# Optimization experiments

Hardware: AMD Instinct MI355X
Metric: run time of the kernel (lower is better)

Reference implementation:

```python
import jax, jax.numpy as jnp
import numpy as np

NUM_HEADS = 16
HEAD_DIM = 64

def setup_inputs() -> dict:
    key = jax.random.key(0)
    k1, k2, k3 = jax.random.split(key, 3)
    B, S, H = 2, 2048, 1024
    inner = NUM_HEADS * HEAD_DIM  # 1024
    x = jax.random.normal(k1, (B, S, H), dtype=jnp.float32)
    w_qkv = jax.random.normal(k2, (H, 3 * inner), dtype=jnp.float32) * (1.0 / np.sqrt(H))
    b_qkv = jnp.zeros((3 * inner,), dtype=jnp.float32)
    w_out = jax.random.normal(k3, (inner, H), dtype=jnp.float32) * (1.0 / np.sqrt(inner))
    b_out = jnp.zeros((H,), dtype=jnp.float32)
    return {"x": x, "w_qkv": w_qkv, "b_qkv": b_qkv, "w_out": w_out, "b_out": b_out}

def reference(x, w_qkv, b_qkv, w_out, b_out):
    B, S, H = x.shape
    nh, hd = NUM_HEADS, HEAD_DIM
    qkv = x @ w_qkv + b_qkv                      # [B,S,3*nh*hd]
    qkv = qkv.reshape(B, S, 3, nh, hd)
    qkv = jnp.transpose(qkv, (2, 0, 3, 1, 4))    # [3,B,nh,S,hd]
    q, k, v = qkv[0], qkv[1], qkv[2]
    scale = jnp.sqrt(jnp.asarray(hd, dtype=x.dtype))
    attn = jnp.einsum('bhqd,bhkd->bhqk', q, k) / scale  # [B,nh,S,S]
    attn = jax.nn.softmax(attn, axis=-1)
    out = jnp.einsum('bhqk,bhkd->bhqd', attn, v)        # [B,nh,S,hd]
    out = jnp.transpose(out, (0, 2, 1, 3)).reshape(B, S, nh * hd)
    out = out @ w_out + b_out                    # [B,S,H]
    return out
```

## Files before the change

### kernel.cpp

```cpp
#include <hip/hip_runtime.h>
#include <stdint.h>

typedef short bf16x8 __attribute__((ext_vector_type(8)));
typedef float f32x4 __attribute__((ext_vector_type(4)));

#if __has_builtin(__builtin_amdgcn_exp2f)
#define EXP2F(x) __builtin_amdgcn_exp2f(x)
#else
#define EXP2F(x) exp2f(x)
#endif

#define QSCALE 0.18033688011112042f

__device__ __forceinline__ unsigned short f2bf(float f) {
  unsigned u = __float_as_uint(f);
  u += 0x7fffu + ((u >> 16) & 1u);
  return (unsigned short)(u >> 16);
}

__device__ __forceinline__ unsigned cvtpk(float lo, float hi) {
  unsigned r;
  asm("v_cvt_pk_bf16_f32 %0, %1, %2" : "=v"(r) : "v"(lo), "v"(hi));
  return r;
}

__device__ __forceinline__ void gld16(const ushort* g, ushort* l) {
  __builtin_amdgcn_global_load_lds(
      (__attribute__((address_space(1))) void*)g,
      (__attribute__((address_space(3))) void*)l, 16, 0, 0);
}

__global__ __launch_bounds__(256) void k_cast_bf16(const float* __restrict__ in,
                                                   ushort* __restrict__ out) {
  int i = (blockIdx.x * 256 + threadIdx.x) * 8;
  float4 a = *(const float4*)(in + i);
  float4 b = *(const float4*)(in + i + 4);
  union { ushort u[8]; uint4 q; } r;
  r.u[0] = f2bf(a.x); r.u[1] = f2bf(a.y); r.u[2] = f2bf(a.z); r.u[3] = f2bf(a.w);
  r.u[4] = f2bf(b.x); r.u[5] = f2bf(b.y); r.u[6] = f2bf(b.z); r.u[7] = f2bf(b.w);
  *(uint4*)(out + i) = r.q;
}

__global__ __launch_bounds__(256) void k_transpose_cast(const float* __restrict__ in,
                                                        ushort* __restrict__ out,
                                                        int R, int C) {
  __shared__ float tl[32][33];
  int t = threadIdx.x;
  {
    int r = t >> 3, c4 = (t & 7) * 4;
    float4 v = *(const float4*)(in + (size_t)(blockIdx.y * 32 + r) * C + blockIdx.x * 32 + c4);
    tl[r][c4] = v.x; tl[r][c4 + 1] = v.y; tl[r][c4 + 2] = v.z; tl[r][c4 + 3] = v.w;
  }
  __syncthreads();
  {
    int c = t >> 3, r4 = (t & 7) * 4;
    union { ushort u[4]; uint2 q; } o;
    o.u[0] = f2bf(tl[r4][c]);     o.u[1] = f2bf(tl[r4 + 1][c]);
    o.u[2] = f2bf(tl[r4 + 2][c]); o.u[3] = f2bf(tl[r4 + 3][c]);
    *(uint2*)(out + (size_t)(blockIdx.x * 32 + c) * R + blockIdx.y * 32 + r4) = o.q;
  }
}

__global__ __launch_bounds__(256) void k_vtrans(const ushort* __restrict__ V,
                                                ushort* __restrict__ Vt) {
  __shared__ ushort tl[64 * 72];
  int t = threadIdx.x;
  const ushort* inp = V + (size_t)blockIdx.y * 131072 + blockIdx.x * 4096;
#pragma unroll
  for (int p = 0; p < 2; ++p) {
    int r = (t >> 3) + p * 32, c8 = (t & 7) * 8;
    *(uint4*)&tl[r * 72 + c8] = *(const uint4*)&inp[r * 64 + c8];
  }
  __syncthreads();
  ushort* outp = Vt + (size_t)blockIdx.y * 131072 + blockIdx.x * 64;
#pragma unroll
  for (int p = 0; p < 2; ++p) {
    int d = (t >> 3) + p * 32, s8 = (t & 7) * 8;
    union { ushort u[8]; uint4 q; } o;
#pragma unroll
    for (int j = 0; j < 8; ++j) o.u[j] = tl[(s8 + j) * 72 + d];
    *(uint4*)&outp[d * 2048 + s8] = o.q;
  }
}

template <int MODE>
__global__ __launch_bounds__(256, 2) void k_gemm(
    const ushort* __restrict__ A, const ushort* __restrict__ Bt,
    const float* __restrict__ bias, ushort* __restrict__ Q,
    ushort* __restrict__ Ko, ushort* __restrict__ V, float* __restrict__ Out) {
  __shared__ ushort As[128 * 32];
  __shared__ ushort Bs[128 * 32];
  const int t = threadIdx.x;
  const int lane = t & 63, wid = t >> 6;
  const int wr = wid >> 1, wc = wid & 1;
  const int rt = blockIdx.y, ct = blockIdx.x;

  const int srow = t >> 2, sslot = t & 3;
  const ushort* ga = A + (size_t)(rt * 128 + srow) * 1024 + sslot * 8;
  const ushort* gb = Bt + (size_t)(ct * 128 + srow) * 1024 + sslot * 8;
  ushort* lA = &As[t * 8];
  ushort* lB = &Bs[t * 8];

  f32x4 acc[4][4];
#pragma unroll
  for (int m = 0; m < 4; ++m)
#pragma unroll
    for (int n = 0; n < 4; ++n) acc[m][n] = (f32x4){0.f, 0.f, 0.f, 0.f};

  int aidx[4], bidx[4];
#pragma unroll
  for (int m = 0; m < 4; ++m) {
    int ra = wr * 64 + m * 16 + (lane & 15);
    aidx[m] = ra * 32 + ((lane >> 4) << 3);
    int rb = wc * 64 + m * 16 + (lane & 15);
    bidx[m] = rb * 32 + ((lane >> 4) << 3);
  }

  gld16(ga, lA); gld16(ga + 65536, lA + 2048);
  gld16(gb, lB); gld16(gb + 65536, lB + 2048);

  for (int kt = 0; kt < 32; ++kt) {
    __syncthreads();
    bf16x8 af[4], bfv[4];
#pragma unroll
    for (int m = 0; m < 4; ++m) af[m] = *(const bf16x8*)&As[aidx[m]];
#pragma unroll
    for (int n = 0; n < 4; ++n) bfv[n] = *(const bf16x8*)&Bs[bidx[n]];
    __syncthreads();
    if (kt < 31) {
      const ushort* ga2 = ga + (kt + 1) * 32;
      const ushort* gb2 = gb + (kt + 1) * 32;
      gld16(ga2, lA); gld16(ga2 + 65536, lA + 2048);
      gld16(gb2, lB); gld16(gb2 + 65536, lB + 2048);
    }
#pragma unroll
    for (int m = 0; m < 4; ++m)
#pragma unroll
      for (int n = 0; n < 4; ++n)
        acc[m][n] = __builtin_amdgcn_mfma_f32_16x16x32_bf16(af[m], bfv[n], acc[m][n], 0, 0, 0);
  }

  const int colb = ct * 128 + wc * 64;
  const int rowb = rt * 128 + wr * 64;
  if constexpr (MODE == 0) {
#pragma unroll
    for (int n = 0; n < 4; ++n) {
      int col = colb + n * 16 + (lane & 15);
      float bv = bias[col];
      int three = col >> 10, hx = (col >> 6) & 15, d = col & 63;
      float sc = (three == 0) ? QSCALE : 1.0f;
      ushort* dst = (three == 0) ? Q : (three == 1) ? Ko : V;
#pragma unroll
      for (int m = 0; m < 4; ++m) {
        int r0 = rowb + m * 16 + ((lane >> 4) << 2);
#pragma unroll
        for (int r = 0; r < 4; ++r) {
          int row = r0 + r;
          int b = row >> 11, s = row & 2047;
          dst[(size_t)((b * 16 + hx) * 2048 + s) * 64 + d] = f2bf((acc[m][n][r] + bv) * sc);
        }
      }
    }
  } else {
#pragma unroll
    for (int n = 0; n < 4; ++n) {
      int col = colb + n * 16 + (lane & 15);
      float bv = bias[col];
#pragma unroll
      for (int m = 0; m < 4; ++m) {
        int r0 = rowb + m * 16 + ((lane >> 4) << 2);
#pragma unroll
        for (int r = 0; r < 4; ++r)
          Out[(size_t)(r0 + r) * 1024 + col] = acc[m][n][r] + bv;
      }
    }
  }
}

__global__ __launch_bounds__(512, 2) void k_attn(const ushort* __restrict__ Qb,
                                                 const ushort* __restrict__ Kb,
                                                 const ushort* __restrict__ Vtb,
                                                 ushort* __restrict__ AO) {
  __shared__ ushort Ks[2][64 * 72];
  __shared__ ushort Vs[2][64 * 72];
  __shared__ ushort Ps[128 * 64];
  const int t = threadIdx.x, lane = t & 63, wid = t >> 6;
  const int c = lane & 15, g = lane >> 4;
  const int bh = blockIdx.y, qt = blockIdx.x;
  const ushort* Qh = Qb + (size_t)bh * 131072;
  const ushort* Kh = Kb + (size_t)bh * 131072;
  const ushort* Vh = Vtb + (size_t)bh * 131072;

  bf16x8 qf[2];
#pragma unroll
  for (int kk = 0; kk < 2; ++kk) {
    int row = qt * 128 + wid * 16 + c;
    qf[kk] = *(const bf16x8*)&Qh[row * 64 + kk * 32 + g * 8];
  }

  f32x4 oacc[4];
#pragma unroll
  for (int n = 0; n < 4; ++n) oacc[n] = (f32x4){0.f, 0.f, 0.f, 0.f};
  float mrow = -1e30f, lpart = 0.f;

  const int strow = t >> 3, stcol = (t & 7) * 8;
  const int stoff = strow * 72 + stcol;

  int kidx[4][2];
#pragma unroll
  for (int n = 0; n < 4; ++n)
#pragma unroll
    for (int kk = 0; kk < 2; ++kk)
      kidx[n][kk] = (n * 16 + c) * 72 + (kk * 4 + g) * 8;

  const int prow = wid * 16 + c;
  const int keyu = (c & 14) << 2;
  int psw[4], prd[2];
#pragma unroll
  for (int n = 0; n < 4; ++n) psw[n] = prow * 64 + ((n * 16 + g * 4) ^ keyu);
#pragma unroll
  for (int kk = 0; kk < 2; ++kk) prd[kk] = prow * 64 + ((kk * 32 + g * 8) ^ keyu);

  uint4 kreg = *(const uint4*)&Kh[(size_t)strow * 64 + stcol];
  uint4 vreg = *(const uint4*)&Vh[(size_t)strow * 2048 + stcol];
  *(uint4*)&Ks[0][stoff] = kreg;
  *(uint4*)&Vs[0][stoff] = vreg;
  kreg = *(const uint4*)&Kh[(size_t)(64 + strow) * 64 + stcol];
  vreg = *(const uint4*)&Vh[(size_t)strow * 2048 + 64 + stcol];
  __syncthreads();

  int cur = 0;
  for (int kt = 0; kt < 32; ++kt) {
    const ushort* Kc = &Ks[cur][0];
    const ushort* Vc = &Vs[cur][0];
    f32x4 sacc[4];
#pragma unroll
    for (int n = 0; n < 4; ++n) sacc[n] = (f32x4){0.f, 0.f, 0.f, 0.f};
    __builtin_amdgcn_s_setprio(1);
#pragma unroll
    for (int kk = 0; kk < 2; ++kk)
#pragma unroll
      for (int n = 0; n < 4; ++n) {
        bf16x8 kf = *(const bf16x8*)&Kc[kidx[n][kk]];
        sacc[n] = __builtin_amdgcn_mfma_f32_16x16x32_bf16(kf, qf[kk], sacc[n], 0, 0, 0);
      }
    __builtin_amdgcn_s_setprio(0);
    float mx0 = fmaxf(fmaxf(sacc[0][0], sacc[0][1]), fmaxf(sacc[0][2], sacc[0][3]));
    float mx1 = fmaxf(fmaxf(sacc[1][0], sacc[1][1]), fmaxf(sacc[1][2], sacc[1][3]));
    float mx2 = fmaxf(fmaxf(sacc[2][0], sacc[2][1]), fmaxf(sacc[2][2], sacc[2][3]));
    float mx3 = fmaxf(fmaxf(sacc[3][0], sacc[3][1]), fmaxf(sacc[3][2], sacc[3][3]));
    float mx = fmaxf(fmaxf(mx0, mx1), fmaxf(mx2, mx3));
    mx = fmaxf(mx, __shfl_xor(mx, 16));
    mx = fmaxf(mx, __shfl_xor(mx, 32));
    if (!__all(mx <= mrow + 12.0f)) {
      float mo = mrow;
      float mn = fmaxf(mo, mx);
      float corr = EXP2F(mo - mn);
      mrow = mn;
      lpart *= corr;
#pragma unroll
      for (int r = 0; r < 4; ++r) {
        float cr = __shfl(corr, (g << 2) + r);
        oacc[0][r] *= cr; oacc[1][r] *= cr; oacc[2][r] *= cr; oacc[3][r] *= cr;
      }
    }
    const float mu = mrow;
    float p[4][4];
#pragma unroll
    for (int n = 0; n < 4; ++n)
#pragma unroll
      for (int r = 0; r < 4; ++r) p[n][r] = EXP2F(sacc[n][r] - mu);
    lpart += ((p[0][0] + p[0][1]) + (p[0][2] + p[0][3])) +
             ((p[1][0] + p[1][1]) + (p[1][2] + p[1][3])) +
             ((p[2][0] + p[2][1]) + (p[2][2] + p[2][3])) +
             ((p[3][0] + p[3][1]) + (p[3][2] + p[3][3]));
#pragma unroll
    for (int n = 0; n < 4; ++n) {
      uint2 w;
      w.x = cvtpk(p[n][0], p[n][1]);
      w.y = cvtpk(p[n][2], p[n][3]);
      *(uint2*)&Ps[psw[n]] = w;
    }
    __builtin_amdgcn_s_setprio(1);
#pragma unroll
    for (int kk = 0; kk < 2; ++kk) {
      bf16x8 pa = *(const bf16x8*)&Ps[prd[kk]];
#pragma unroll
      for (int nd = 0; nd < 4; ++nd) {
        bf16x8 vf = *(const bf16x8*)&Vc[kidx[nd][kk]];
        oacc[nd] = __builtin_amdgcn_mfma_f32_16x16x32_bf16(pa, vf, oacc[nd], 0, 0, 0);
      }
    }
    __builtin_amdgcn_s_setprio(0);
    if (kt < 31) {
      *(uint4*)&Ks[cur ^ 1][stoff] = kreg;
      *(uint4*)&Vs[cur ^ 1][stoff] = vreg;
      if (kt < 30) {
        kreg = *(const uint4*)&Kh[(size_t)((kt + 2) * 64 + strow) * 64 + stcol];
        vreg = *(const uint4*)&Vh[(size_t)strow * 2048 + (kt + 2) * 64 + stcol];
      }
    }
    __syncthreads();
    cur ^= 1;
  }

  const int b = bh >> 4, h = bh & 15;
  lpart += __shfl_xor(lpart, 16);
  lpart += __shfl_xor(lpart, 32);
  float inv = 1.0f / lpart;
  float invr[4];
#pragma unroll
  for (int r = 0; r < 4; ++r) invr[r] = __shfl(inv, (g << 2) + r);
#pragma unroll
  for (int nd = 0; nd < 4; ++nd) {
    int d = nd * 16 + c;
#pragma unroll
    for (int r = 0; r < 4; ++r) {
      int s = qt * 128 + wid * 16 + (g << 2) + r;
      AO[(size_t)((b * 2048 + s) * 16 + h) * 64 + d] = f2bf(oacc[nd][r] * invr[r]);
    }
  }
}

extern "C" void kernel_launch(void* const* d_in, const int* in_sizes, int n_in,
                              void* d_out, int out_size, void* d_ws, size_t ws_size,
                              hipStream_t stream) {
  const float* x = (const float*)d_in[0];
  const float* w_qkv = (const float*)d_in[1];
  const float* b_qkv = (const float*)d_in[2];
  const float* w_out = (const float*)d_in[3];
  const float* b_out = (const float*)d_in[4];
  float* out = (float*)d_out;

  char* p = (char*)d_ws;
  ushort* xb = (ushort*)p;    p += (size_t)4096 * 1024 * 2;
  ushort* wqkvT = (ushort*)p; p += (size_t)3072 * 1024 * 2;
  ushort* woutT = (ushort*)p; p += (size_t)1024 * 1024 * 2;
  ushort* Qb = (ushort*)p;    p += (size_t)32 * 2048 * 64 * 2;
  ushort* Kb = (ushort*)p;    p += (size_t)32 * 2048 * 64 * 2;
  ushort* Vb = (ushort*)p;    p += (size_t)32 * 2048 * 64 * 2;
  ushort* Vtb = (ushort*)p;   p += (size_t)32 * 2048 * 64 * 2;
  ushort* AO = xb;

  k_cast_bf16<<<2048, 256, 0, stream>>>(x, xb);
  k_transpose_cast<<<dim3(96, 32), 256, 0, stream>>>(w_qkv, wqkvT, 1024, 3072);
  k_transpose_cast<<<dim3(32, 32), 256, 0, stream>>>(w_out, woutT, 1024, 1024);
  k_gemm<0><<<dim3(24, 32), 256, 0, stream>>>(xb, wqkvT, b_qkv, Qb, Kb, Vb, nullptr);
  k_vtrans<<<dim3(32, 32), 256, 0, stream>>>(Vb, Vtb);
  k_attn<<<dim3(16, 32), 512, 0, stream>>>(Qb, Kb, Vtb, AO);
  k_gemm<1><<<dim3(8, 32), 256, 0, stream>>>(AO, woutT, b_out, nullptr, nullptr, nullptr, out);
}
```

Measured before the change: 134.6 us.

## Process two query tiles per wave and keep P in registers via permlane swaps

The attention kernel now runs 4 waves per block, each handling 32 query rows (two 16-row tiles), instead of 8 waves with 16 rows each. Each K/V fragment read from LDS is therefore reused across two MFMAs. The softmax probabilities no longer go through LDS; they are rearranged into the MFMA A-operand layout in registers using v_permlane32/16_swap. This cuts LDS traffic and removes the P staging buffer, at the cost of more VGPRs per wave and fewer waves per block to hide latency.

```diff
diff --git a/kernel.cpp b/kernel.cpp
--- a/kernel.cpp
+++ b/kernel.cpp
@@ -22,6 +22,13 @@
   unsigned r;
   asm("v_cvt_pk_bf16_f32 %0, %1, %2" : "=v"(r) : "v"(lo), "v"(hi));
   return r;
+}
+
+__device__ __forceinline__ void pl32(unsigned& a, unsigned& b) {
+  asm("v_permlane32_swap_b32 %0, %1" : "+v"(a), "+v"(b));
+}
+__device__ __forceinline__ void pl16(unsigned& a, unsigned& b) {
+  asm("v_permlane16_swap_b32 %0, %1" : "+v"(a), "+v"(b));
 }
 
 __device__ __forceinline__ void gld16(const ushort* g, ushort* l) {
@@ -177,13 +184,12 @@
   }
 }
 
-__global__ __launch_bounds__(512, 2) void k_attn(const ushort* __restrict__ Qb,
+__global__ __launch_bounds__(256, 2) void k_attn(const ushort* __restrict__ Qb,
                                                  const ushort* __restrict__ Kb,
                                                  const ushort* __restrict__ Vtb,
                                                  ushort* __restrict__ AO) {
   __shared__ ushort Ks[2][64 * 72];
   __shared__ ushort Vs[2][64 * 72];
-  __shared__ ushort Ps[128 * 64];
   const int t = threadIdx.x, lane = t & 63, wid = t >> 6;
   const int c = lane & 15, g = lane >> 4;
   const int bh = blockIdx.y, qt = blockIdx.x;
@@ -191,19 +197,23 @@
   const ushort* Kh = Kb + (size_t)bh * 131072;
   const ushort* Vh = Vtb + (size_t)bh * 131072;
 
-  bf16x8 qf[2];
-#pragma unroll
-  for (int kk = 0; kk < 2; ++kk) {
-    int row = qt * 128 + wid * 16 + c;
-    qf[kk] = *(const bf16x8*)&Qh[row * 64 + kk * 32 + g * 8];
-  }
-
-  f32x4 oacc[4];
-#pragma unroll
-  for (int n = 0; n < 4; ++n) oacc[n] = (f32x4){0.f, 0.f, 0.f, 0.f};
-  float mrow = -1e30f, lpart = 0.f;
-
-  const int strow = t >> 3, stcol = (t & 7) * 8;
+  bf16x8 qf[2][2];
+#pragma unroll
+  for (int cb = 0; cb < 2; ++cb)
+#pragma unroll
+    for (int kk = 0; kk < 2; ++kk) {
+      int row = qt * 128 + wid * 32 + cb * 16 + c;
+      qf[cb][kk] = *(const bf16x8*)&Qh[row * 64 + kk * 32 + g * 8];
+    }
+
+  f32x4 oacc[2][4];
+#pragma unroll
+  for (int cb = 0; cb < 2; ++cb)
+#pragma unroll
+    for (int n = 0; n < 4; ++n) oacc[cb][n] = (f32x4){0.f, 0.f, 0.f, 0.f};
+  float mrow[2] = {-1e30f, -1e30f}, lpart[2] = {0.f, 0.f};
+
+  const int strow = t >> 2, stcol = (t & 3) * 16;
   const int stoff = strow * 72 + stcol;
 
   int kidx[4][2];
@@ -213,91 +223,106 @@
     for (int kk = 0; kk < 2; ++kk)
       kidx[n][kk] = (n * 16 + c) * 72 + (kk * 4 + g) * 8;
 
-  const int prow = wid * 16 + c;
-  const int keyu = (c & 14) << 2;
-  int psw[4], prd[2];
-#pragma unroll
-  for (int n = 0; n < 4; ++n) psw[n] = prow * 64 + ((n * 16 + g * 4) ^ keyu);
-#pragma unroll
-  for (int kk = 0; kk < 2; ++kk) prd[kk] = prow * 64 + ((kk * 32 + g * 8) ^ keyu);
-
-  uint4 kreg = *(const uint4*)&Kh[(size_t)strow * 64 + stcol];
-  uint4 vreg = *(const uint4*)&Vh[(size_t)strow * 2048 + stcol];
-  *(uint4*)&Ks[0][stoff] = kreg;
-  *(uint4*)&Vs[0][stoff] = vreg;
-  kreg = *(const uint4*)&Kh[(size_t)(64 + strow) * 64 + stcol];
-  vreg = *(const uint4*)&Vh[(size_t)strow * 2048 + 64 + stcol];
+  uint4 kr0 = *(const uint4*)&Kh[(size_t)strow * 64 + stcol];
+  uint4 kr1 = *(const uint4*)&Kh[(size_t)strow * 64 + stcol + 8];
+  uint4 vr0 = *(const uint4*)&Vh[(size_t)strow * 2048 + stcol];
+  uint4 vr1 = *(const uint4*)&Vh[(size_t)strow * 2048 + stcol + 8];
+  *(uint4*)&Ks[0][stoff] = kr0; *(uint4*)&Ks[0][stoff + 8] = kr1;
+  *(uint4*)&Vs[0][stoff] = vr0; *(uint4*)&Vs[0][stoff + 8] = vr1;
+  kr0 = *(const uint4*)&Kh[(size_t)(64 + strow) * 64 + stcol];
+  kr1 = *(const uint4*)&Kh[(size_t)(64 + strow) * 64 + stcol + 8];
+  vr0 = *(const uint4*)&Vh[(size_t)strow * 2048 + 64 + stcol];
+  vr1 = *(const uint4*)&Vh[(size_t)strow * 2048 + 64 + stcol + 8];
   __syncthreads();
 
   int cur = 0;
   for (int kt = 0; kt < 32; ++kt) {
     const ushort* Kc = &Ks[cur][0];
     const ushort* Vc = &Vs[cur][0];
-    f32x4 sacc[4];
-#pragma unroll
-    for (int n = 0; n < 4; ++n) sacc[n] = (f32x4){0.f, 0.f, 0.f, 0.f};
+    f32x4 sacc[2][4];
+#pragma unroll
+    for (int cb = 0; cb < 2; ++cb)
+#pragma unroll
+      for (int n = 0; n < 4; ++n) sacc[cb][n] = (f32x4){0.f, 0.f, 0.f, 0.f};
     __builtin_amdgcn_s_setprio(1);
 #pragma unroll
     for (int kk = 0; kk < 2; ++kk)
 #pragma unroll
       for (int n = 0; n < 4; ++n) {
         bf16x8 kf = *(const bf16x8*)&Kc[kidx[n][kk]];
-        sacc[n] = __builtin_amdgcn_mfma_f32_16x16x32_bf16(kf, qf[kk], sacc[n], 0, 0, 0);
+        sacc[0][n] = __builtin_amdgcn_mfma_f32_16x16x32_bf16(kf, qf[0][kk], sacc[0][n], 0, 0, 0);
+        sacc[1][n] = __builtin_amdgcn_mfma_f32_16x16x32_bf16(kf, qf[1][kk], sacc[1][n], 0, 0, 0);
       }
     __builtin_amdgcn_s_setprio(0);
-    float mx0 = fmaxf(fmaxf(sacc[0][0], sacc[0][1]), fmaxf(sacc[0][2], sacc[0][3]));
-    float mx1 = fmaxf(fmaxf(sacc[1][0], sacc[1][1]), fmaxf(sacc[1][2], sacc[1][3]));
-    float mx2 = fmaxf(fmaxf(sacc[2][0], sacc[2][1]), fmaxf(sacc[2][2], sacc[2][3]));
-    float mx3 = fmaxf(fmaxf(sacc[3][0], sacc[3][1]), fmaxf(sacc[3][2], sacc[3][3]));
-    float mx = fmaxf(fmaxf(mx0, mx1), fmaxf(mx2, mx3));
-    mx = fmaxf(mx, __shfl_xor(mx, 16));
-    mx = fmaxf(mx, __shfl_xor(mx, 32));
-    if (!__all(mx <= mrow + 12.0f)) {
-      float mo = mrow;
-      float mn = fmaxf(mo, mx);
-      float corr = EXP2F(mo - mn);
-      mrow = mn;
-      lpart *= corr;
-#pragma unroll
-      for (int r = 0; r < 4; ++r) {
-        float cr = __shfl(corr, (g << 2) + r);
-        oacc[0][r] *= cr; oacc[1][r] *= cr; oacc[2][r] *= cr; oacc[3][r] *= cr;
-      }
-    }
-    const float mu = mrow;
-    float p[4][4];
-#pragma unroll
-    for (int n = 0; n < 4; ++n)
-#pragma unroll
-      for (int r = 0; r < 4; ++r) p[n][r] = EXP2F(sacc[n][r] - mu);
-    lpart += ((p[0][0] + p[0][1]) + (p[0][2] + p[0][3])) +
-             ((p[1][0] + p[1][1]) + (p[1][2] + p[1][3])) +
-             ((p[2][0] + p[2][1]) + (p[2][2] + p[2][3])) +
-             ((p[3][0] + p[3][1]) + (p[3][2] + p[3][3]));
-#pragma unroll
-    for (int n = 0; n < 4; ++n) {
-      uint2 w;
-      w.x = cvtpk(p[n][0], p[n][1]);
-      w.y = cvtpk(p[n][2], p[n][3]);
-      *(uint2*)&Ps[psw[n]] = w;
+    uint2 W[2][4];
+#pragma unroll
+    for (int cb = 0; cb < 2; ++cb) {
+      float mx0 = fmaxf(fmaxf(sacc[cb][0][0], sacc[cb][0][1]), fmaxf(sacc[cb][0][2], sacc[cb][0][3]));
+      float mx1 = fmaxf(fmaxf(sacc[cb][1][0], sacc[cb][1][1]), fmaxf(sacc[cb][1][2], sacc[cb][1][3]));
+      float mx2 = fmaxf(fmaxf(sacc[cb][2][0], sacc[cb][2][1]), fmaxf(sacc[cb][2][2], sacc[cb][2][3]));
+      float mx3 = fmaxf(fmaxf(sacc[cb][3][0], sacc[cb][3][1]), fmaxf(sacc[cb][3][2], sacc[cb][3][3]));
+      float mx = fmaxf(fmaxf(mx0, mx1), fmaxf(mx2, mx3));
+      mx = fmaxf(mx, __shfl_xor(mx, 16));
+      mx = fmaxf(mx, __shfl_xor(mx, 32));
+      if (!__all(mx <= mrow[cb] + 12.0f)) {
+        float mo = mrow[cb];
+        float mn = fmaxf(mo, mx);
+        float corr = EXP2F(mo - mn);
+        mrow[cb] = mn;
+        lpart[cb] *= corr;
+#pragma unroll
+        for (int r = 0; r < 4; ++r) {
+          float cr = __shfl(corr, (g << 2) + r);
+          oacc[cb][0][r] *= cr; oacc[cb][1][r] *= cr;
+          oacc[cb][2][r] *= cr; oacc[cb][3][r] *= cr;
+        }
+      }
+      const float mu = mrow[cb];
+      float ps = lpart[cb];
+#pragma unroll
+      for (int n = 0; n < 4; ++n) {
+        float p0 = EXP2F(sacc[cb][n][0] - mu);
+        float p1 = EXP2F(sacc[cb][n][1] - mu);
+        float p2 = EXP2F(sacc[cb][n][2] - mu);
+        float p3 = EXP2F(sacc[cb][n][3] - mu);
+        ps += (p0 + p1) + (p2 + p3);
+        W[cb][n].x = cvtpk(p0, p1);
+        W[cb][n].y = cvtpk(p2, p3);
+      }
+      lpart[cb] = ps;
     }
     __builtin_amdgcn_s_setprio(1);
 #pragma unroll
     for (int kk = 0; kk < 2; ++kk) {
-      bf16x8 pa = *(const bf16x8*)&Ps[prd[kk]];
+      bf16x8 paf[2];
+#pragma unroll
+      for (int cb = 0; cb < 2; ++cb) {
+        unsigned a0 = W[cb][2 * kk].x, b0 = W[cb][2 * kk + 1].x;
+        pl32(a0, b0); pl16(a0, b0);
+        unsigned a1 = W[cb][2 * kk].y, b1 = W[cb][2 * kk + 1].y;
+        pl32(a1, b1); pl16(a1, b1);
+        union { unsigned u[4]; bf16x8 v; } fr;
+        fr.u[0] = a0; fr.u[1] = a1; fr.u[2] = b0; fr.u[3] = b1;
+        paf[cb] = fr.v;
+      }
 #pragma unroll
       for (int nd = 0; nd < 4; ++nd) {
         bf16x8 vf = *(const bf16x8*)&Vc[kidx[nd][kk]];
-        oacc[nd] = __builtin_amdgcn_mfma_f32_16x16x32_bf16(pa, vf, oacc[nd], 0, 0, 0);
+        oacc[0][nd] = __builtin_amdgcn_mfma_f32_16x16x32_bf16(paf[0], vf, oacc[0][nd], 0, 0, 0);
+        oacc[1][nd] = __builtin_amdgcn_mfma_f32_16x16x32_bf16(paf[1], vf, oacc[1][nd], 0, 0, 0);
       }
     }
     __builtin_amdgcn_s_setprio(0);
     if (kt < 31) {
-      *(uint4*)&Ks[cur ^ 1][stoff] = kreg;
-      *(uint4*)&Vs[cur ^ 1][stoff] = vreg;
+      ushort* kd = &Ks[cur ^ 1][stoff];
+      *(uint4*)kd = kr0; *(uint4*)(kd + 8) = kr1;
+      ushort* vd = &Vs[cur ^ 1][stoff];
+      *(uint4*)vd = vr0; *(uint4*)(vd + 8) = vr1;
       if (kt < 30) {
-        kreg = *(const uint4*)&Kh[(size_t)((kt + 2) * 64 + strow) * 64 + stcol];
-        vreg = *(const uint4*)&Vh[(size_t)strow * 2048 + (kt + 2) * 64 + stcol];
+        const ushort* gk = &Kh[(size_t)((kt + 2) * 64 + strow) * 64 + stcol];
+        kr0 = *(const uint4*)gk; kr1 = *(const uint4*)(gk + 8);
+        const ushort* gv = &Vh[(size_t)strow * 2048 + (kt + 2) * 64 + stcol];
+        vr0 = *(const uint4*)gv; vr1 = *(const uint4*)(gv + 8);
       }
     }
     __syncthreads();
@@ -305,19 +330,23 @@
   }
 
   const int b = bh >> 4, h = bh & 15;
-  lpart += __shfl_xor(lpart, 16);
-  lpart += __shfl_xor(lpart, 32);
-  float inv = 1.0f / lpart;
-  float invr[4];
-#pragma unroll
-  for (int r = 0; r < 4; ++r) invr[r] = __shfl(inv, (g << 2) + r);
-#pragma unroll
-  for (int nd = 0; nd < 4; ++nd) {
-    int d = nd * 16 + c;
-#pragma unroll
-    for (int r = 0; r < 4; ++r) {
-      int s = qt * 128 + wid * 16 + (g << 2) + r;
-      AO[(size_t)((b * 2048 + s) * 16 + h) * 64 + d] = f2bf(oacc[nd][r] * invr[r]);
+#pragma unroll
+  for (int cb = 0; cb < 2; ++cb) {
+    float lp = lpart[cb];
+    lp += __shfl_xor(lp, 16);
+    lp += __shfl_xor(lp, 32);
+    float inv = 1.0f / lp;
+    float invr[4];
+#pragma unroll
+    for (int r = 0; r < 4; ++r) invr[r] = __shfl(inv, (g << 2) + r);
+#pragma unroll
+    for (int nd = 0; nd < 4; ++nd) {
+      int d = nd * 16 + c;
+#pragma unroll
+      for (int r = 0; r < 4; ++r) {
+        int s = qt * 128 + wid * 32 + cb * 16 + (g << 2) + r;
+        AO[(size_t)((b * 2048 + s) * 16 + h) * 64 + d] = f2bf(oacc[cb][nd][r] * invr[r]);
+      }
     }
   }
 }
@@ -347,6 +376,6 @@
   k_transpose_cast<<<dim3(32, 32), 256, 0, stream>>>(w_out, woutT, 1024, 1024);
   k_gemm<0><<<dim3(24, 32), 256, 0, stream>>>(xb, wqkvT, b_qkv, Qb, Kb, Vb, nullptr);
   k_vtrans<<<dim3(32, 32), 256, 0, stream>>>(Vb, Vtb);
-  k_attn<<<dim3(16, 32), 512, 0, stream>>>(Qb, Kb, Vtb, AO);
+  k_attn<<<dim3(16, 32), 256, 0, stream>>>(Qb, Kb, Vtb, AO);
   k_gemm<1><<<dim3(8, 32), 256, 0, stream>>>(AO, woutT, b_out, nullptr, nullptr, nullptr, out);
 }
```

Result: faster. 130.4 us (-3.1%).

## Keep P in registers via permlane swaps and halve attention block size

Applied to the files above, without the earlier changes.

The softmax probabilities are no longer round-tripped through a shared-memory Ps buffer. They are rearranged into the MFMA A-operand layout in registers using v_permlane32/16_swap instructions. The attention block shrinks from 512 to 256 threads (64 query rows), which doubles the grid and has each thread stage two 16-byte chunks of K/V. This removes LDS writes and reads for P and frees LDS, but each block's K/V tile is reused by half as many queries, so global and L2 traffic for K/V doubles.

```diff
diff --git a/kernel.cpp b/kernel.cpp
--- a/kernel.cpp
+++ b/kernel.cpp
@@ -22,6 +22,13 @@
   unsigned r;
   asm("v_cvt_pk_bf16_f32 %0, %1, %2" : "=v"(r) : "v"(lo), "v"(hi));
   return r;
+}
+
+__device__ __forceinline__ void pl32(unsigned& a, unsigned& b) {
+  asm("v_permlane32_swap_b32 %0, %1" : "+v"(a), "+v"(b));
+}
+__device__ __forceinline__ void pl16(unsigned& a, unsigned& b) {
+  asm("v_permlane16_swap_b32 %0, %1" : "+v"(a), "+v"(b));
 }
 
 __device__ __forceinline__ void gld16(const ushort* g, ushort* l) {
@@ -177,13 +184,12 @@
   }
 }
 
-__global__ __launch_bounds__(512, 2) void k_attn(const ushort* __restrict__ Qb,
+__global__ __launch_bounds__(256, 2) void k_attn(const ushort* __restrict__ Qb,
                                                  const ushort* __restrict__ Kb,
                                                  const ushort* __restrict__ Vtb,
                                                  ushort* __restrict__ AO) {
   __shared__ ushort Ks[2][64 * 72];
   __shared__ ushort Vs[2][64 * 72];
-  __shared__ ushort Ps[128 * 64];
   const int t = threadIdx.x, lane = t & 63, wid = t >> 6;
   const int c = lane & 15, g = lane >> 4;
   const int bh = blockIdx.y, qt = blockIdx.x;
@@ -194,7 +200,7 @@
   bf16x8 qf[2];
 #pragma unroll
   for (int kk = 0; kk < 2; ++kk) {
-    int row = qt * 128 + wid * 16 + c;
+    int row = qt * 64 + wid * 16 + c;
     qf[kk] = *(const bf16x8*)&Qh[row * 64 + kk * 32 + g * 8];
   }
 
@@ -203,7 +209,7 @@
   for (int n = 0; n < 4; ++n) oacc[n] = (f32x4){0.f, 0.f, 0.f, 0.f};
   float mrow = -1e30f, lpart = 0.f;
 
-  const int strow = t >> 3, stcol = (t & 7) * 8;
+  const int strow = t >> 2, stcol = (t & 3) * 16;
   const int stoff = strow * 72 + stcol;
 
   int kidx[4][2];
@@ -213,20 +219,16 @@
     for (int kk = 0; kk < 2; ++kk)
       kidx[n][kk] = (n * 16 + c) * 72 + (kk * 4 + g) * 8;
 
-  const int prow = wid * 16 + c;
-  const int keyu = (c & 14) << 2;
-  int psw[4], prd[2];
-#pragma unroll
-  for (int n = 0; n < 4; ++n) psw[n] = prow * 64 + ((n * 16 + g * 4) ^ keyu);
-#pragma unroll
-  for (int kk = 0; kk < 2; ++kk) prd[kk] = prow * 64 + ((kk * 32 + g * 8) ^ keyu);
-
-  uint4 kreg = *(const uint4*)&Kh[(size_t)strow * 64 + stcol];
-  uint4 vreg = *(const uint4*)&Vh[(size_t)strow * 2048 + stcol];
-  *(uint4*)&Ks[0][stoff] = kreg;
-  *(uint4*)&Vs[0][stoff] = vreg;
-  kreg = *(const uint4*)&Kh[(size_t)(64 + strow) * 64 + stcol];
-  vreg = *(const uint4*)&Vh[(size_t)strow * 2048 + 64 + stcol];
+  uint4 kr0 = *(const uint4*)&Kh[(size_t)strow * 64 + stcol];
+  uint4 kr1 = *(const uint4*)&Kh[(size_t)strow * 64 + stcol + 8];
+  uint4 vr0 = *(const uint4*)&Vh[(size_t)strow * 2048 + stcol];
+  uint4 vr1 = *(const uint4*)&Vh[(size_t)strow * 2048 + stcol + 8];
+  *(uint4*)&Ks[0][stoff] = kr0; *(uint4*)&Ks[0][stoff + 8] = kr1;
+  *(uint4*)&Vs[0][stoff] = vr0; *(uint4*)&Vs[0][stoff + 8] = vr1;
+  kr0 = *(const uint4*)&Kh[(size_t)(64 + strow) * 64 + stcol];
+  kr1 = *(const uint4*)&Kh[(size_t)(64 + strow) * 64 + stcol + 8];
+  vr0 = *(const uint4*)&Vh[(size_t)strow * 2048 + 64 + stcol];
+  vr1 = *(const uint4*)&Vh[(size_t)strow * 2048 + 64 + stcol + 8];
   __syncthreads();
 
   int cur = 0;
@@ -265,39 +267,47 @@
       }
     }
     const float mu = mrow;
-    float p[4][4];
-#pragma unroll
-    for (int n = 0; n < 4; ++n)
-#pragma unroll
-      for (int r = 0; r < 4; ++r) p[n][r] = EXP2F(sacc[n][r] - mu);
-    lpart += ((p[0][0] + p[0][1]) + (p[0][2] + p[0][3])) +
-             ((p[1][0] + p[1][1]) + (p[1][2] + p[1][3])) +
-             ((p[2][0] + p[2][1]) + (p[2][2] + p[2][3])) +
-             ((p[3][0] + p[3][1]) + (p[3][2] + p[3][3]));
-#pragma unroll
-    for (int n = 0; n < 4; ++n) {
-      uint2 w;
-      w.x = cvtpk(p[n][0], p[n][1]);
-      w.y = cvtpk(p[n][2], p[n][3]);
-      *(uint2*)&Ps[psw[n]] = w;
+    uint2 W[4];
+    {
+      float ps = lpart;
+#pragma unroll
+      for (int n = 0; n < 4; ++n) {
+        float p0 = EXP2F(sacc[n][0] - mu);
+        float p1 = EXP2F(sacc[n][1] - mu);
+        float p2 = EXP2F(sacc[n][2] - mu);
+        float p3 = EXP2F(sacc[n][3] - mu);
+        ps += (p0 + p1) + (p2 + p3);
+        W[n].x = cvtpk(p0, p1);
+        W[n].y = cvtpk(p2, p3);
+      }
+      lpart = ps;
     }
     __builtin_amdgcn_s_setprio(1);
 #pragma unroll
     for (int kk = 0; kk < 2; ++kk) {
-      bf16x8 pa = *(const bf16x8*)&Ps[prd[kk]];
+      unsigned a0 = W[2 * kk].x, b0 = W[2 * kk + 1].x;
+      pl32(a0, b0); pl16(a0, b0);
+      unsigned a1 = W[2 * kk].y, b1 = W[2 * kk + 1].y;
+      pl32(a1, b1); pl16(a1, b1);
+      union { unsigned u[4]; bf16x8 v; } fr;
+      fr.u[0] = a0; fr.u[1] = a1; fr.u[2] = b0; fr.u[3] = b1;
 #pragma unroll
       for (int nd = 0; nd < 4; ++nd) {
         bf16x8 vf = *(const bf16x8*)&Vc[kidx[nd][kk]];
-        oacc[nd] = __builtin_amdgcn_mfma_f32_16x16x32_bf16(pa, vf, oacc[nd], 0, 0, 0);
+        oacc[nd] = __builtin_amdgcn_mfma_f32_16x16x32_bf16(fr.v, vf, oacc[nd], 0, 0, 0);
       }
     }
     __builtin_amdgcn_s_setprio(0);
     if (kt < 31) {
-      *(uint4*)&Ks[cur ^ 1][stoff] = kreg;
-      *(uint4*)&Vs[cur ^ 1][stoff] = vreg;
+      ushort* kd = &Ks[cur ^ 1][stoff];
+      *(uint4*)kd = kr0; *(uint4*)(kd + 8) = kr1;
+      ushort* vd = &Vs[cur ^ 1][stoff];
+      *(uint4*)vd = vr0; *(uint4*)(vd + 8) = vr1;
       if (kt < 30) {
-        kreg = *(const uint4*)&Kh[(size_t)((kt + 2) * 64 + strow) * 64 + stcol];
-        vreg = *(const uint4*)&Vh[(size_t)strow * 2048 + (kt + 2) * 64 + stcol];
+        kr0 = *(const uint4*)&Kh[(size_t)((kt + 2) * 64 + strow) * 64 + stcol];
+        kr1 = *(const uint4*)&Kh[(size_t)((kt + 2) * 64 + strow) * 64 + stcol + 8];
+        vr0 = *(const uint4*)&Vh[(size_t)strow * 2048 + (kt + 2) * 64 + stcol];
+        vr1 = *(const uint4*)&Vh[(size_t)strow * 2048 + (kt + 2) * 64 + stcol + 8];
       }
     }
     __syncthreads();
@@ -316,7 +326,7 @@
     int d = nd * 16 + c;
 #pragma unroll
     for (int r = 0; r < 4; ++r) {
-      int s = qt * 128 + wid * 16 + (g << 2) + r;
+      int s = qt * 64 + wid * 16 + (g << 2) + r;
       AO[(size_t)((b * 2048 + s) * 16 + h) * 64 + d] = f2bf(oacc[nd][r] * invr[r]);
     }
   }
@@ -347,6 +357,6 @@
   k_transpose_cast<<<dim3(32, 32), 256, 0, stream>>>(w_out, woutT, 1024, 1024);
   k_gemm<0><<<dim3(24, 32), 256, 0, stream>>>(xb, wqkvT, b_qkv, Qb, Kb, Vb, nullptr);
   k_vtrans<<<dim3(32, 32), 256, 0, stream>>>(Vb, Vtb);
-  k_attn<<<dim3(16, 32), 512, 0, stream>>>(Qb, Kb, Vtb, AO);
+  k_attn<<<dim3(32, 32), 256, 0, stream>>>(Qb, Kb, Vtb, AO);
   k_gemm<1><<<dim3(8, 32), 256, 0, stream>>>(AO, woutT, b_out, nullptr, nullptr, nullptr, out);
 }
```

New measurement: 134.9 us. About the same (+0.2%).
